# Kernel tuning notes

Hardware: AMD Instinct MI355X
Metric: run time of the kernel (lower is better)

Reference implementation:

```python
import jax, jax.numpy as jnp
import numpy as np

N = 50000      # nodes
E = 800000     # edges
C = 64         # in_channels
H = 192        # hidden_channels
ED = 16        # edge_dim
G = 2048       # num graphs (molecules)
L_EXTRA = 2    # num_layers - 1
T = 2          # num_timesteps
NEG0 = 0.2     # GATConv default negative_slope (first conv)
NEG = 0.01     # later convs / mol conv


def setup_inputs() -> dict:
    ks = iter(jax.random.split(jax.random.key(0), 48))
    def rn(shape, s=0.05):
        return jax.random.normal(next(ks), shape, dtype=jnp.float32) * s
    z = lambda *s: jnp.zeros(s, jnp.float32)
    return {
        "x": jax.random.normal(next(ks), (N, C), dtype=jnp.float32),
        "edge_index": jax.random.randint(next(ks), (2, E), 0, N),
        "edge_attr": jax.random.normal(next(ks), (E, ED), dtype=jnp.float32),
        "batch": jnp.sort(jax.random.randint(next(ks), (N,), 0, G)),
        "lin1_W": rn((H, C)), "lin1_b": z(H),
        "conv0_W": rn((H, H)), "conv0_att_s": rn((H,)), "conv0_att_d": rn((H,)),
        "conv0_We": rn((H, ED)), "conv0_att_e": rn((H,)), "conv0_b": z(H),
        "convs_W": rn((L_EXTRA, H, H)), "convs_att_s": rn((L_EXTRA, H)),
        "convs_att_d": rn((L_EXTRA, H)), "convs_b": z(L_EXTRA, H),
        "gru_Wih": rn((L_EXTRA + 1, 3 * H, H)), "gru_Whh": rn((L_EXTRA + 1, 3 * H, H)),
        "gru_bih": z(L_EXTRA + 1, 3 * H), "gru_bhh": z(L_EXTRA + 1, 3 * H),
        "mol_Wsrc": rn((H, H)), "mol_Wdst": rn((H, H)),
        "mol_att_s": rn((H,)), "mol_att_d": rn((H,)), "mol_b": z(H),
        "mgru_Wih": rn((3 * H, H)), "mgru_Whh": rn((3 * H, H)),
        "mgru_bih": z(3 * H), "mgru_bhh": z(3 * H),
        "lin2_W": rn((1, H)), "lin2_b": z(1),
    }


def _lrelu(v, slope):
    return jnp.where(v >= 0, v, slope * v)


def _seg_softmax(alpha, dst, n_seg):
    m = jax.ops.segment_max(alpha, dst, num_segments=n_seg)
    m = jnp.where(jnp.isfinite(m), m, 0.0)           # empty segments -> 0
    e = jnp.exp(alpha - m[dst])
    s = jax.ops.segment_sum(e, dst, num_segments=n_seg)
    return e / (s[dst] + 1e-16)


def _gat(h_src, h_dst, src, dst, att_s, att_d, b, slope, n_dst, alpha_extra=None):
    # h_src/h_dst are already linearly transformed node features
    alpha = (h_src * att_s).sum(-1)[src] + (h_dst * att_d).sum(-1)[dst]
    if alpha_extra is not None:
        alpha = alpha + alpha_extra
    w = _seg_softmax(_lrelu(alpha, slope), dst, n_dst)     # scatter-softmax over dst
    return jax.ops.segment_sum(h_src[src] * w[:, None], dst, num_segments=n_dst) + b


def _gru(h, hx, Wih, Whh, bih, bhh):
    gi = h @ Wih.T + bih
    gh = hx @ Whh.T + bhh
    ir, iz, inn = jnp.split(gi, 3, axis=-1)
    hr, hz, hn = jnp.split(gh, 3, axis=-1)
    r = jax.nn.sigmoid(ir + hr)
    zz = jax.nn.sigmoid(iz + hz)
    n = jnp.tanh(inn + r * hn)
    return (1.0 - zz) * n + zz * hx


def reference(x, edge_index, edge_attr, batch,
              lin1_W, lin1_b,
              conv0_W, conv0_att_s, conv0_att_d, conv0_We, conv0_att_e, conv0_b,
              convs_W, convs_att_s, convs_att_d, convs_b,
              gru_Wih, gru_Whh, gru_bih, gru_bhh,
              mol_Wsrc, mol_Wdst, mol_att_s, mol_att_d, mol_b,
              mgru_Wih, mgru_Whh, mgru_bih, mgru_bhh,
              lin2_W, lin2_b):
    src, dst = edge_index[0], edge_index[1]
    x = _lrelu(x @ lin1_W.T + lin1_b, 0.01)            # F.leaky_relu_ (slope 0.01)

    # ---- first GATConv: edge features + self loops (fill_value='mean') ----
    loop = jnp.arange(N)
    src0 = jnp.concatenate([src, loop])
    dst0 = jnp.concatenate([dst, loop])
    ea0 = jnp.concatenate([edge_attr, jnp.broadcast_to(edge_attr.mean(0), (N, ED))], 0)
    hW = x @ conv0_W.T                                  # shared lin_src/lin_dst
    alpha_e = (ea0 @ conv0_We.T * conv0_att_e).sum(-1)  # [E+N]
    h = jax.nn.elu(_gat(hW, hW, src0, dst0, conv0_att_s, conv0_att_d,
                        conv0_b, NEG0, N, alpha_e))
    x = jax.nn.relu(_gru(h, x, gru_Wih[0], gru_Whh[0], gru_bih[0], gru_bhh[0]))

    # ---- remaining atom GATConv + GRU layers ----
    for l in range(L_EXTRA):
        hW = x @ convs_W[l].T
        h = jax.nn.elu(_gat(hW, hW, src, dst, convs_att_s[l], convs_att_d[l],
                            convs_b[l], NEG, N))
        x = jax.nn.relu(_gru(h, x, gru_Wih[l + 1], gru_Whh[l + 1],
                             gru_bih[l + 1], gru_bhh[l + 1]))

    # ---- molecule readout: bipartite GAT (nodes -> molecules) + GRU ----
    out = jax.nn.relu(jax.ops.segment_sum(x, batch, num_segments=G))  # global_add_pool
    hs = x @ mol_Wsrc.T                                 # src transform (x fixed)
    node_ids = jnp.arange(N)
    for _ in range(T):
        hd = out @ mol_Wdst.T
        h = jax.nn.elu(_gat(hs, hd, node_ids, batch, mol_att_s, mol_att_d,
                            mol_b, NEG, G))
        out = jax.nn.relu(_gru(h, out, mgru_Wih, mgru_Whh, mgru_bih, mgru_bhh))

    return out @ lin2_W.T + lin2_b                      # [G, 1]
```

## Files before the change

kernel.cpp:

```cpp
#include <hip/hip_runtime.h>
#include <math.h>

#define NN    50000
#define EE    800000
#define CIN   64
#define HH    192
#define EDIM  16
#define GG    2048
#define H3    576
#define EA_BLOCKS 256
#define FRAG_ELEMS (36 * 6 * 64)
#define G4_WLAYER 221184

typedef _Float16 f16;
typedef _Float16 half8 __attribute__((ext_vector_type(8)));
typedef float f32x4 __attribute__((ext_vector_type(4)));

__device__ __forceinline__ unsigned fmap(float f) {
    unsigned u = __float_as_uint(f);
    return (u & 0x80000000u) ? ~u : (u | 0x80000000u);
}
__device__ __forceinline__ float funmap(unsigned u) {
    if (u == 0u) return 0.0f;
    return (u & 0x80000000u) ? __uint_as_float(u ^ 0x80000000u)
                             : __uint_as_float(~u);
}

__device__ __forceinline__ float fast_exp(float x) {
    return __builtin_amdgcn_exp2f(1.442695041f * x);
}
__device__ __forceinline__ float fast_sig(float x) {
    return __builtin_amdgcn_rcpf(1.f + __builtin_amdgcn_exp2f(-1.442695041f * x));
}
__device__ __forceinline__ float fast_tanh(float x) {
    return 1.f - 2.f * __builtin_amdgcn_rcpf(1.f + __builtin_amdgcn_exp2f(2.885390082f * x));
}
__device__ __forceinline__ float fast_expm1(float x) {
    return __builtin_amdgcn_exp2f(1.442695041f * x) - 1.f;
}

__device__ __forceinline__ void gload_lds16(const f16* g, f16* l) {
    __builtin_amdgcn_global_load_lds(
        (const __attribute__((address_space(1))) unsigned int*)g,
        (__attribute__((address_space(3))) unsigned int*)l,
        16, 0, 0);
}

__global__ void cvt_f2h(const float* __restrict__ s, f16* __restrict__ d, int n)
{
    int i = blockIdx.x * blockDim.x + threadIdx.x;
    if (i < n) d[i] = (f16)s[i];
}

struct Cvt8 { const float* s[8]; f16* d[8]; int n[8]; };
__global__ void cvt_multi(Cvt8 c)
{
    int slot = blockIdx.y;
    int i = blockIdx.x * blockDim.x + threadIdx.x;
    if (i < c.n[slot]) c.d[slot][i] = (f16)c.s[slot][i];
}

struct Pack8 { const f16* s[8]; f16* d[8]; };
__global__ __launch_bounds__(256) void pack_frag(Pack8 p)
{
    int slot = blockIdx.y;
    int idx = blockIdx.x * 256 + threadIdx.x;
    if (idx >= FRAG_ELEMS) return;
    int cb   = idx / 384;
    int rem  = idx % 384;
    int c    = rem / 64;
    int lane = rem % 64;
    int col = cb * 16 + (lane & 15);
    int k   = c * 32 + (lane >> 4) * 8;
    *(half8*)(p.d[slot] + (size_t)idx * 8) =
        *(const half8*)(p.s[slot] + (size_t)col * 192 + k);
}

__global__ __launch_bounds__(256) void pack4(const f16* __restrict__ Wih,
                                             const f16* __restrict__ Whh,
                                             f16* __restrict__ out)
{
    int layer = blockIdx.y;
    int idx = blockIdx.x * 256 + threadIdx.x;
    if (idx >= 27648) return;
    int frag = idx >> 6, lane = idx & 63;
    int pc6 = frag / 24, r24 = frag % 24;
    int p = pc6 / 6, c = pc6 % 6;
    int m = r24 / 12, g = (r24 % 12) >> 2, cb = r24 & 3;
    const f16* srcm = (m == 0 ? Wih : Whh) + (size_t)layer * (H3 * HH);
    int col = g * 192 + p * 64 + cb * 16 + (lane & 15);
    int k   = c * 32 + (lane >> 4) * 8;
    *(half8*)(out + (size_t)layer * G4_WLAYER + (size_t)idx * 8) =
        *(const half8*)(srcm + (size_t)col * 192 + k);
}

__global__ void hist_kernel(const int* __restrict__ idx, int* __restrict__ deg, int n, int nbins)
{
    int i = blockIdx.x * blockDim.x + threadIdx.x;
    if (i < n) {
        unsigned b = (unsigned)idx[i];
        if (b < (unsigned)nbins) atomicAdd(&deg[b], 1);
    }
}

__global__ void scan_wave(const int* __restrict__ deg, int* __restrict__ rowptr,
                          unsigned* __restrict__ cursor, int n)
{
    int lane = threadIdx.x & 63;
    int carry = 0;
    for (int base = 0; base < n; base += 64) {
        int i = base + lane;
        int v = (i < n) ? deg[i] : 0;
        int x = v;
        #pragma unroll
        for (int off = 1; off < 64; off <<= 1) {
            int t = __shfl_up(x, off);
            if (lane >= off) x += t;
        }
        int ex = carry + x - v;
        if (i < n) {
            rowptr[i] = ex;
            if (cursor) cursor[i] = (unsigned)ex;
        }
        carry += __shfl(x, 63);
    }
    if (lane == 0) rowptr[n] = carry;
}

__global__ __launch_bounds__(256) void chunk_sum(const int* __restrict__ deg,
                                                 int* __restrict__ csum, int n)
{
    int base = blockIdx.x * 1024;
    int tid = threadIdx.x;
    int i0 = base + tid * 4;
    int s = 0;
    #pragma unroll
    for (int k = 0; k < 4; k++) { int i = i0 + k; if (i < n) s += deg[i]; }
    #pragma unroll
    for (int off = 32; off > 0; off >>= 1) s += __shfl_down(s, off);
    __shared__ int ws[4];
    int lane = tid & 63, w = tid >> 6;
    if (lane == 0) ws[w] = s;
    __syncthreads();
    if (tid == 0) csum[blockIdx.x] = ws[0] + ws[1] + ws[2] + ws[3];
}

__global__ __launch_bounds__(256) void local_scan(const int* __restrict__ deg,
                                                  const int* __restrict__ choff,
                                                  int* __restrict__ rowptr,
                                                  unsigned* __restrict__ cursor,
                                                  int n, int nchunks)
{
    int base = blockIdx.x * 1024;
    int tid = threadIdx.x;
    int lane = tid & 63, w = tid >> 6;
    int i0 = base + tid * 4;
    int v[4];
    #pragma unroll
    for (int k = 0; k < 4; k++) { int i = i0 + k; v[k] = (i < n) ? deg[i] : 0; }
    int tsum = v[0] + v[1] + v[2] + v[3];
    int x = tsum;
    #pragma unroll
    for (int off = 1; off < 64; off <<= 1) {
        int t = __shfl_up(x, off);
        if (lane >= off) x += t;
    }
    __shared__ int wtot[4];
    if (lane == 63) wtot[w] = x;
    __syncthreads();
    int woff = 0;
    #pragma unroll
    for (int j = 0; j < 4; j++) if (j < w) woff += wtot[j];
    int ex = choff[blockIdx.x] + woff + x - tsum;
    #pragma unroll
    for (int k = 0; k < 4; k++) {
        int i = i0 + k;
        if (i < n) {
            rowptr[i] = ex;
            if (cursor) cursor[i] = (unsigned)ex;
        }
        ex += v[k];
    }
    if (blockIdx.x == 0 && tid == 0) rowptr[n] = choff[nchunks];
}

__global__ void scatter_kernel(const int* __restrict__ src, const int* __restrict__ dst,
                               unsigned* __restrict__ cursor,
                               int* __restrict__ csr_src, int* __restrict__ csr_eid, int E)
{
    int e = blockIdx.x * blockDim.x + threadIdx.x;
    if (e >= E) return;
    unsigned d = (unsigned)dst[e];
    if (d >= (unsigned)NN) return;
    unsigned p = atomicAdd(&cursor[d], 1u);
    if (p < (unsigned)E) {
        csr_src[p] = src[e];
        csr_eid[p] = e;
    }
}

__global__ __launch_bounds__(256) void gemm_mfma(const f16* __restrict__ A,
                                                 const f16* __restrict__ W,
                                                 const float* __restrict__ bias,
                                                 float* __restrict__ Cf,
                                                 f16* __restrict__ Ch,
                                                 int M, int N, int K, int act)
{
    __shared__ __align__(16) f16 sA[64 * 40];
    const int tid  = threadIdx.x;
    const int lane = tid & 63;
    const int wid  = tid >> 6;
    const int wy = wid >> 1, wx = wid & 1;
    const int m0 = blockIdx.x << 6, n0 = blockIdx.y << 6;
    const int n_ = lane & 15, quad = lane >> 4;

    f32x4 acc[2][2] = {};
    int boff0 = (n0 + wx * 32 + n_) * K + quad * 8;
    int boff1 = boff0 + 16 * K;

    const int srow = tid >> 2;
    const int skc  = (tid & 3) << 3;

    for (int k0 = 0; k0 < K; k0 += 32) {
        half8 av = {};
        int gm = m0 + srow;
        if (gm < M) av = *(const half8*)(A + (size_t)gm * K + k0 + skc);
        *(half8*)(sA + srow * 40 + skc) = av;
        __syncthreads();
        half8 a0 = *(const half8*)(sA + (wy * 32 + n_) * 40 + quad * 8);
        half8 a1 = *(const half8*)(sA + (wy * 32 + 16 + n_) * 40 + quad * 8);
        half8 b0 = *(const half8*)(W + boff0 + k0);
        half8 b1 = *(const half8*)(W + boff1 + k0);
        acc[0][0] = __builtin_amdgcn_mfma_f32_16x16x32_f16(a0, b0, acc[0][0], 0, 0, 0);
        acc[0][1] = __builtin_amdgcn_mfma_f32_16x16x32_f16(a0, b1, acc[0][1], 0, 0, 0);
        acc[1][0] = __builtin_amdgcn_mfma_f32_16x16x32_f16(a1, b0, acc[1][0], 0, 0, 0);
        acc[1][1] = __builtin_amdgcn_mfma_f32_16x16x32_f16(a1, b1, acc[1][1], 0, 0, 0);
        __syncthreads();
    }
    #pragma unroll
    for (int i = 0; i < 2; i++)
        #pragma unroll
        for (int j = 0; j < 2; j++) {
            int col = n0 + wx * 32 + j * 16 + n_;
            float bv = bias ? bias[col] : 0.f;
            #pragma unroll
            for (int reg = 0; reg < 4; reg++) {
                int row = m0 + wy * 32 + i * 16 + quad * 4 + reg;
                if (row >= M) continue;
                float v = acc[i][j][reg] + bv;
                if (act == 1) v = v >= 0.f ? v : 0.01f * v;
                if (Cf) Cf[(size_t)row * N + col] = v;
                if (Ch) Ch[(size_t)row * N + col] = (f16)v;
            }
        }
}

#define GRU_LDP 208
__global__ __launch_bounds__(256, 2) void gru_mfma(const f16* __restrict__ H16,
                                                   f16* __restrict__ X16,
                                                   const f16* __restrict__ Pih,
                                                   const f16* __restrict__ Phh,
                                                   const float* __restrict__ bih,
                                                   const float* __restrict__ bhh,
                                                   int M)
{
    __shared__ __align__(16) f16 sH[32 * GRU_LDP];
    __shared__ __align__(16) f16 sX[32 * GRU_LDP];
    const int tid  = threadIdx.x;
    const int lane = tid & 63;
    const int w    = tid >> 6;
    const int n_ = lane & 15, quad = lane >> 4;
    const int node0 = blockIdx.x << 5;

    {
        const int r  = tid >> 3;
        const int cb = (tid & 7) * 24;
        const int gm = node0 + r;
        if (gm < M) {
            const f16* hp = H16 + (size_t)gm * 192 + cb;
            const f16* xp = X16 + (size_t)gm * 192 + cb;
            #pragma unroll
            for (int q = 0; q < 3; q++) {
                *(half8*)(sH + r * GRU_LDP + cb + q * 8) = *(const half8*)(hp + q * 8);
                *(half8*)(sX + r * GRU_LDP + cb + q * 8) = *(const half8*)(xp + q * 8);
            }
        } else {
            half8 z = {};
            #pragma unroll
            for (int q = 0; q < 3; q++) {
                *(half8*)(sH + r * GRU_LDP + cb + q * 8) = z;
                *(half8*)(sX + r * GRU_LDP + cb + q * 8) = z;
            }
        }
    }
    __syncthreads();

    f32x4 aRZ[2][2][3] = {};
    f32x4 aIN[2][3] = {};
    f32x4 aHN[2][3] = {};
    int fb[3][3];
    #pragma unroll
    for (int g = 0; g < 3; g++)
        #pragma unroll
        for (int t = 0; t < 3; t++)
            fb[g][t] = (g * 12 + w * 3 + t) * 3072 + lane * 8;

    #pragma unroll 1
    for (int c = 0; c < 6; c++) {
        int k0 = c * 32;
        int po = c * 512;
        half8 ah0 = *(const half8*)(sH + n_ * GRU_LDP + k0 + quad * 8);
        half8 ah1 = *(const half8*)(sH + (16 + n_) * GRU_LDP + k0 + quad * 8);
        half8 ax0 = *(const half8*)(sX + n_ * GRU_LDP + k0 + quad * 8);
        half8 ax1 = *(const half8*)(sX + (16 + n_) * GRU_LDP + k0 + quad * 8);
        #pragma unroll
        for (int g = 0; g < 2; g++)
            #pragma unroll
            for (int t = 0; t < 3; t++) {
                half8 bI = *(const half8*)(Pih + fb[g][t] + po);
                half8 bH = *(const half8*)(Phh + fb[g][t] + po);
                aRZ[0][g][t] = __builtin_amdgcn_mfma_f32_16x16x32_f16(ah0, bI, aRZ[0][g][t], 0, 0, 0);
                aRZ[1][g][t] = __builtin_amdgcn_mfma_f32_16x16x32_f16(ah1, bI, aRZ[1][g][t], 0, 0, 0);
                aRZ[0][g][t] = __builtin_amdgcn_mfma_f32_16x16x32_f16(ax0, bH, aRZ[0][g][t], 0, 0, 0);
                aRZ[1][g][t] = __builtin_amdgcn_mfma_f32_16x16x32_f16(ax1, bH, aRZ[1][g][t], 0, 0, 0);
            }
        #pragma unroll
        for (int t = 0; t < 3; t++) {
            half8 bI = *(const half8*)(Pih + fb[2][t] + po);
            half8 bH = *(const half8*)(Phh + fb[2][t] + po);
            aIN[0][t] = __builtin_amdgcn_mfma_f32_16x16x32_f16(ah0, bI, aIN[0][t], 0, 0, 0);
            aIN[1][t] = __builtin_amdgcn_mfma_f32_16x16x32_f16(ah1, bI, aIN[1][t], 0, 0, 0);
            aHN[0][t] = __builtin_amdgcn_mfma_f32_16x16x32_f16(ax0, bH, aHN[0][t], 0, 0, 0);
            aHN[1][t] = __builtin_amdgcn_mfma_f32_16x16x32_f16(ax1, bH, aHN[1][t], 0, 0, 0);
        }
    }

    #pragma unroll
    for (int t = 0; t < 3; t++) {
        const int c0 = w * 48 + t * 16 + n_;
        float brz = bih[c0] + bhh[c0];
        float bzz = bih[c0 + 192] + bhh[c0 + 192];
        float bin = bih[c0 + 384], bhn = bhh[c0 + 384];
        #pragma unroll
        for (int half = 0; half < 2; half++) {
            #pragma unroll
            for (int reg = 0; reg < 4; reg++) {
                int rl = half * 16 + quad * 4 + reg;
                int node = node0 + rl;
                if (node >= M) continue;
                float hx = (float)sX[rl * GRU_LDP + c0];
                float r  = fast_sig(aRZ[half][0][t][reg] + brz);
                float z  = fast_sig(aRZ[half][1][t][reg] + bzz);
                float nn = fast_tanh(aIN[half][t][reg] + bin + r * (aHN[half][t][reg] + bhn));
                float o  = (1.f - z) * nn + z * hx;
                X16[(size_t)node * 192 + c0] = (f16)(o > 0.f ? o : 0.f);
            }
        }
    }
}

#define G4_ROWS 128
__global__ __launch_bounds__(256, 2) void gru4_mfma(const f16* __restrict__ H16,
                                                    const f16* __restrict__ Xold,
                                                    f16* __restrict__ Xnew,
                                                    const f16* __restrict__ W4,
                                                    const float* __restrict__ bih,
                                                    const float* __restrict__ bhh,
                                                    int M)
{
    __shared__ __align__(16) f16 sB[2][12288];
    const int tid  = threadIdx.x;
    const int lane = tid & 63;
    const int w    = tid >> 6;
    const int n_ = lane & 15, quad = lane >> 4;
    const int rb = blockIdx.x * G4_ROWS + w * 32;
    const int r0 = min(rb + n_,      M - 1);
    const int r1 = min(rb + 16 + n_, M - 1);

    half8 aA[4], aB[4];
    f32x4 acc[2][4][4] = {};

#define G4_STAGE(B, PC) do {                                                   \
        const f16* gs_ = W4 + (size_t)(PC) * 12288 + (w * 6) * 512 + lane * 8; \
        f16* ls_ = &sB[B][(w * 6) * 512];                                      \
        _Pragma("unroll")                                                      \
        for (int i_ = 0; i_ < 6; i_++)                                         \
            gload_lds16(gs_ + i_ * 512, ls_ + i_ * 512);                       \
    } while (0)

#define G4_ALOAD(AB, C) do {                                                   \
        const f16* h0_ = H16  + (size_t)r0 * 192 + (C) * 32 + quad * 8;        \
        const f16* h1_ = H16  + (size_t)r1 * 192 + (C) * 32 + quad * 8;        \
        const f16* x0_ = Xold + (size_t)r0 * 192 + (C) * 32 + quad * 8;        \
        const f16* x1_ = Xold + (size_t)r1 * 192 + (C) * 32 + quad * 8;        \
        AB[0] = *(const half8*)h0_;                                            \
        AB[1] = *(const half8*)h1_;                                            \
        AB[2] = *(const half8*)x0_;                                            \
        AB[3] = *(const half8*)x1_;                                            \
    } while (0)

#define G4_COMP(AB, CUR) do {                                                  \
        _Pragma("unroll")                                                      \
        for (int cb_ = 0; cb_ < 4; cb_++) {                                    \
            const f16* bp_ = &sB[CUR][cb_ * 512 + lane * 8];                   \
            half8 rI_ = *(const half8*)(bp_);                                  \
            half8 zI_ = *(const half8*)(bp_ + 2048);                           \
            half8 nI_ = *(const half8*)(bp_ + 4096);                           \
            half8 rH_ = *(const half8*)(bp_ + 6144);                           \
            half8 zH_ = *(const half8*)(bp_ + 8192);                           \
            half8 nH_ = *(const half8*)(bp_ + 10240);                          \
            acc[0][cb_][0] = __builtin_amdgcn_mfma_f32_16x16x32_f16(AB[0], rI_, acc[0][cb_][0], 0, 0, 0); \
            acc[0][cb_][0] = __builtin_amdgcn_mfma_f32_16x16x32_f16(AB[2], rH_, acc[0][cb_][0], 0, 0, 0); \
            acc[1][cb_][0] = __builtin_amdgcn_mfma_f32_16x16x32_f16(AB[1], rI_, acc[1][cb_][0], 0, 0, 0); \
            acc[1][cb_][0] = __builtin_amdgcn_mfma_f32_16x16x32_f16(AB[3], rH_, acc[1][cb_][0], 0, 0, 0); \
            acc[0][cb_][1] = __builtin_amdgcn_mfma_f32_16x16x32_f16(AB[0], zI_, acc[0][cb_][1], 0, 0, 0); \
            acc[0][cb_][1] = __builtin_amdgcn_mfma_f32_16x16x32_f16(AB[2], zH_, acc[0][cb_][1], 0, 0, 0); \
            acc[1][cb_][1] = __builtin_amdgcn_mfma_f32_16x16x32_f16(AB[1], zI_, acc[1][cb_][1], 0, 0, 0); \
            acc[1][cb_][1] = __builtin_amdgcn_mfma_f32_16x16x32_f16(AB[3], zH_, acc[1][cb_][1], 0, 0, 0); \
            acc[0][cb_][2] = __builtin_amdgcn_mfma_f32_16x16x32_f16(AB[0], nI_, acc[0][cb_][2], 0, 0, 0); \
            acc[1][cb_][2] = __builtin_amdgcn_mfma_f32_16x16x32_f16(AB[1], nI_, acc[1][cb_][2], 0, 0, 0); \
            acc[0][cb_][3] = __builtin_amdgcn_mfma_f32_16x16x32_f16(AB[2], nH_, acc[0][cb_][3], 0, 0, 0); \
            acc[1][cb_][3] = __builtin_amdgcn_mfma_f32_16x16x32_f16(AB[3], nH_, acc[1][cb_][3], 0, 0, 0); \
        }                                                                      \
    } while (0)

#define G4_EPI(P) do {                                                         \
        _Pragma("unroll")                                                      \
        for (int cb_ = 0; cb_ < 4; cb_++) {                                    \
            int c0_ = (P) * 64 + cb_ * 16 + n_;                                \
            float brz_ = bih[c0_] + bhh[c0_];                                  \
            float bzz_ = bih[c0_ + 192] + bhh[c0_ + 192];                      \
            float bin_ = bih[c0_ + 384], bhn_ = bhh[c0_ + 384];                \
            _Pragma("unroll")                                                  \
            for (int rh_ = 0; rh_ < 2; rh_++) {                                \
                _Pragma("unroll")                                              \
                for (int rg_ = 0; rg_ < 4; rg_++) {                            \
                    int node_ = rb + rh_ * 16 + quad * 4 + rg_;                \
                    if (node_ < M) {                                           \
                        float hx_ = (float)Xold[(size_t)node_ * 192 + c0_];    \
                        float r_  = fast_sig(acc[rh_][cb_][0][rg_] + brz_);    \
                        float z_  = fast_sig(acc[rh_][cb_][1][rg_] + bzz_);    \
                        float nn_ = fast_tanh(acc[rh_][cb_][2][rg_] + bin_ + r_ * (acc[rh_][cb_][3][rg_] + bhn_)); \
                        float o_  = (1.f - z_) * nn_ + z_ * hx_;               \
                        Xnew[(size_t)node_ * 192 + c0_] = (f16)(o_ > 0.f ? o_ : 0.f); \
                    }                                                          \
                    acc[rh_][cb_][0][rg_] = 0.f;                               \
                    acc[rh_][cb_][1][rg_] = 0.f;                               \
                    acc[rh_][cb_][2][rg_] = 0.f;                               \
                    acc[rh_][cb_][3][rg_] = 0.f;                               \
                }                                                              \
            }                                                                  \
        }                                                                      \
    } while (0)

#define G4_STEP(ACUR, ANXT, PC) do {                                           \
        if ((PC) < 17) {                                                       \
            G4_STAGE(((PC) + 1) & 1, (PC) + 1);                                \
            G4_ALOAD(ANXT, ((PC) + 1) % 6);                                    \
        }                                                                      \
        G4_COMP(ACUR, (PC) & 1);                                               \
        if (((PC) % 6) == 5) G4_EPI((PC) / 6);                                 \
        __syncthreads();                                                       \
    } while (0)

    G4_STAGE(0, 0);
    G4_ALOAD(aA, 0);
    __syncthreads();

    for (int pc = 0; pc < 18; pc += 2) {
        G4_STEP(aA, aB, pc);
        G4_STEP(aB, aA, pc + 1);
    }

#undef G4_STAGE
#undef G4_ALOAD
#undef G4_COMP
#undef G4_EPI
#undef G4_STEP
}

__global__ void compose_vec2(const float* __restrict__ W, const float* __restrict__ v,
                             float* __restrict__ out, int rows, int cols)
{
    int j = blockIdx.x * 4 + (threadIdx.x >> 6);
    if (j >= cols) return;
    int lane = threadIdx.x & 63;
    float acc = 0.f;
    for (int i = lane; i < rows; i += 64) acc += v[i] * W[(size_t)i * cols + j];
    #pragma unroll
    for (int off = 32; off > 0; off >>= 1) acc += __shfl_down(acc, off);
    if (lane == 0) out[j] = acc;
}

__global__ __launch_bounds__(256) void ea_sum_kernel(const float* __restrict__ ea,
                                                     float* __restrict__ partials, int E)
{
    __shared__ float ws[4][16];
    int tid = threadIdx.x;
    int lane = tid & 63, w = tid >> 6;
    float acc[16];
    #pragma unroll
    for (int f = 0; f < 16; f++) acc[f] = 0.f;
    for (int e = blockIdx.x * blockDim.x + tid; e < E; e += gridDim.x * blockDim.x) {
        const float4* p = (const float4*)(ea + (size_t)e * 16);
        float4 v0 = p[0], v1 = p[1], v2 = p[2], v3 = p[3];
        acc[0] += v0.x; acc[1] += v0.y; acc[2] += v0.z; acc[3] += v0.w;
        acc[4] += v1.x; acc[5] += v1.y; acc[6] += v1.z; acc[7] += v1.w;
        acc[8] += v2.x; acc[9] += v2.y; acc[10] += v2.z; acc[11] += v2.w;
        acc[12] += v3.x; acc[13] += v3.y; acc[14] += v3.z; acc[15] += v3.w;
    }
    #pragma unroll
    for (int off = 32; off > 0; off >>= 1)
        #pragma unroll
        for (int f = 0; f < 16; f++) acc[f] += __shfl_down(acc[f], off);
    if (lane == 0)
        #pragma unroll
        for (int f = 0; f < 16; f++) ws[w][f] = acc[f];
    __syncthreads();
    if (tid < 16)
        partials[blockIdx.x * 16 + tid] = ws[0][tid] + ws[1][tid] + ws[2][tid] + ws[3][tid];
}

__global__ void finalize_aloop(const float* __restrict__ partials, const float* __restrict__ ve,
                               float* __restrict__ aloop, float invE, int nblk)
{
    int tid = threadIdx.x;
    int total = nblk * 16;
    float vf = ve[tid & 15];
    float s = 0.f;
    for (int i = tid; i < total; i += 256) s += partials[i] * vf;
    #pragma unroll
    for (int off = 32; off > 0; off >>= 1) s += __shfl_down(s, off);
    __shared__ float ws[4];
    if ((tid & 63) == 0) ws[tid >> 6] = s;
    __syncthreads();
    if (tid == 0) *aloop = (ws[0] + ws[1] + ws[2] + ws[3]) * invE;
}

__global__ void row_dots_h(const f16* __restrict__ Mat, int M,
                           const float* __restrict__ v1, float* __restrict__ o1,
                           const float* __restrict__ v2, float* __restrict__ o2,
                           const float* __restrict__ bias)
{
    int row = blockIdx.x * 4 + (threadIdx.x >> 6);
    if (row >= M) return;
    int lane = threadIdx.x & 63;
    const f16* rp = Mat + (size_t)row * 192;
    float a1 = 0.f, a2 = 0.f;
    #pragma unroll
    for (int k = 0; k < 3; k++) {
        int f = lane + 64 * k;
        float x = (float)rp[f];
        a1 += x * v1[f];
        if (o2) a2 += x * v2[f];
    }
    #pragma unroll
    for (int off = 32; off > 0; off >>= 1) {
        a1 += __shfl_down(a1, off);
        a2 += __shfl_down(a2, off);
    }
    if (lane == 0) {
        o1[row] = a1 + (bias ? bias[0] : 0.f);
        if (o2) o2[row] = a2;
    }
}

__global__ void edge_alpha_max(const int* __restrict__ srcp, const int* __restrict__ dstp,
                               int E_real, int Etot,
                               const float* __restrict__ as_, const float* __restrict__ ad_,
                               const float* __restrict__ ea, const float* __restrict__ ve,
                               const float* __restrict__ aloop, float slope,
                               float* __restrict__ ab, unsigned* __restrict__ mb)
{
    int i = blockIdx.x * blockDim.x + threadIdx.x;
    if (i >= Etot) return;
    int s_, d_;
    float aext = 0.f;
    if (i < E_real) {
        s_ = srcp ? srcp[i] : i;
        d_ = dstp[i];
        if (ea) {
            const float4* p = (const float4*)(ea + (size_t)i * 16);
            const float4* q = (const float4*)ve;
            float4 e0 = p[0], e1 = p[1], e2 = p[2], e3 = p[3];
            float4 w0 = q[0], w1 = q[1], w2 = q[2], w3 = q[3];
            aext = e0.x * w0.x + e0.y * w0.y + e0.z * w0.z + e0.w * w0.w
                 + e1.x * w1.x + e1.y * w1.y + e1.z * w1.z + e1.w * w1.w
                 + e2.x * w2.x + e2.y * w2.y + e2.z * w2.z + e2.w * w2.w
                 + e3.x * w3.x + e3.y * w3.y + e3.z * w3.z + e3.w * w3.w;
        }
    } else {
        s_ = d_ = i - E_real;
        aext = *aloop;
    }
    float a = as_[s_] + ad_[d_] + aext;
    a = a >= 0.f ? a : slope * a;
    ab[i] = a;
    atomicMax(&mb[d_], fmap(a));
}

__global__ __launch_bounds__(256) void csr_aggregate(const int* __restrict__ rowptr,
                                                     const int* __restrict__ csr_src,
                                                     const int* __restrict__ csr_eid,
                                                     int Ndst, int nF, int nAb,
                                                     int selfloop, int selfAb,
                                                     const float* __restrict__ ab,
                                                     const unsigned* __restrict__ mb,
                                                     const f16* __restrict__ F,
                                                     const float* __restrict__ bias,
                                                     f16* __restrict__ Hout16)
{
    int node = blockIdx.x * 4 + (threadIdx.x >> 6);
    if (node >= Ndst) return;
    int lane = threadIdx.x & 63;
    int start = rowptr[node];
    int deg = rowptr[node + 1] - start;
    deg = min(max(deg, 0), 1 << 20);
    float m = funmap(mb[node]);

    float acc0 = 0.f, acc1 = 0.f, acc2 = 0.f, wsum = 0.f;
    for (int base = 0; base < deg; base += 64) {
        int i = base + lane;
        float wv = 0.f;
        int s = 0;
        if (i < deg) {
            int pos = start + i;
            s = csr_src ? csr_src[pos] : pos;
            if ((unsigned)s >= (unsigned)nF) s = 0;
            unsigned eid = csr_eid ? (unsigned)csr_eid[pos] : (unsigned)pos;
            if (eid >= (unsigned)nAb) eid = 0;
            wv = fast_exp(ab[eid] - m);
        }
        int cnt = min(64, deg - base);
        int j = 0;
        for (; j + 8 <= cnt; j += 8) {
            float wj[8];
            const f16* fp[8];
            #pragma unroll
            for (int q = 0; q < 8; q++) {
                wj[q] = __shfl(wv, j + q);
                fp[q] = F + (size_t)__shfl(s, j + q) * 192;
            }
            float a0[8], a1[8], a2[8];
            #pragma unroll
            for (int q = 0; q < 8; q++) {
                a0[q] = (float)fp[q][lane];
                a1[q] = (float)fp[q][lane + 64];
                a2[q] = (float)fp[q][lane + 128];
            }
            #pragma unroll
            for (int q = 0; q < 8; q++) {
                wsum += wj[q];
                acc0 += wj[q] * a0[q];
                acc1 += wj[q] * a1[q];
                acc2 += wj[q] * a2[q];
            }
        }
        for (; j < cnt; j++) {
            float wj = __shfl(wv, j);
            int   sj = __shfl(s, j);
            const f16* fr = F + (size_t)sj * 192;
            wsum += wj;
            acc0 += wj * (float)fr[lane];
            acc1 += wj * (float)fr[lane + 64];
            acc2 += wj * (float)fr[lane + 128];
        }
    }
    if (selfloop) {
        unsigned eid = (unsigned)(selfAb + node);
        float wv = (eid < (unsigned)nAb) ? fast_exp(ab[eid] - m) : 0.f;
        int s = min(node, nF - 1);
        const f16* fr = F + (size_t)s * 192;
        wsum += wv;
        acc0 += wv * (float)fr[lane];
        acc1 += wv * (float)fr[lane + 64];
        acc2 += wv * (float)fr[lane + 128];
    }
    float inv = 1.f / (wsum + 1e-16f);
    float h0 = acc0 * inv + bias[lane];
    float h1 = acc1 * inv + bias[lane + 64];
    float h2 = acc2 * inv + bias[lane + 128];
    f16* orow = Hout16 + (size_t)node * 192;
    orow[lane]       = (f16)(h0 > 0.f ? h0 : fast_expm1(h0));
    orow[lane + 64]  = (f16)(h1 > 0.f ? h1 : fast_expm1(h1));
    orow[lane + 128] = (f16)(h2 > 0.f ? h2 : fast_expm1(h2));
}

__global__ void pool_csr(const int* __restrict__ brow, const f16* __restrict__ X,
                         f16* __restrict__ outg16, int G)
{
    int g = blockIdx.x * 4 + (threadIdx.x >> 6);
    if (g >= G) return;
    int lane = threadIdx.x & 63;
    float a0 = 0.f, a1 = 0.f, a2 = 0.f;
    int s = max(brow[g], 0);
    int e = min(brow[g + 1], NN);
    for (int n = s; n < e; n++) {
        const f16* xr = X + (size_t)n * 192;
        a0 += (float)xr[lane];
        a1 += (float)xr[lane + 64];
        a2 += (float)xr[lane + 128];
    }
    f16* o = outg16 + (size_t)g * 192;
    o[lane]       = (f16)(a0 > 0.f ? a0 : 0.f);
    o[lane + 64]  = (f16)(a1 > 0.f ? a1 : 0.f);
    o[lane + 128] = (f16)(a2 > 0.f ? a2 : 0.f);
}

extern "C" void kernel_launch(void* const* d_in, const int* in_sizes, int n_in,
                              void* d_out, int out_size, void* d_ws, size_t ws_size,
                              hipStream_t stream)
{
    const float* x_in        = (const float*)d_in[0];
    const int*   ei          = (const int*)  d_in[1];
    const float* eattr       = (const float*)d_in[2];
    const int*   batch       = (const int*)  d_in[3];
    const float* lin1_W      = (const float*)d_in[4];
    const float* lin1_b      = (const float*)d_in[5];
    const float* conv0_W     = (const float*)d_in[6];
    const float* conv0_att_s = (const float*)d_in[7];
    const float* conv0_att_d = (const float*)d_in[8];
    const float* conv0_We    = (const float*)d_in[9];
    const float* conv0_att_e = (const float*)d_in[10];
    const float* conv0_b     = (const float*)d_in[11];
    const float* convs_W     = (const float*)d_in[12];
    const float* convs_att_s = (const float*)d_in[13];
    const float* convs_att_d = (const float*)d_in[14];
    const float* convs_b     = (const float*)d_in[15];
    const float* gru_Wih     = (const float*)d_in[16];
    const float* gru_Whh     = (const float*)d_in[17];
    const float* gru_bih     = (const float*)d_in[18];
    const float* gru_bhh     = (const float*)d_in[19];
    const float* mol_Wsrc    = (const float*)d_in[20];
    const float* mol_Wdst    = (const float*)d_in[21];
    const float* mol_att_s   = (const float*)d_in[22];
    const float* mol_att_d   = (const float*)d_in[23];
    const float* mol_b       = (const float*)d_in[24];
    const float* mgru_Wih    = (const float*)d_in[25];
    const float* mgru_Whh    = (const float*)d_in[26];
    const float* mgru_bih    = (const float*)d_in[27];
    const float* mgru_bhh    = (const float*)d_in[28];
    const float* lin2_W      = (const float*)d_in[29];
    const float* lin2_b      = (const float*)d_in[30];

    const int* src = ei;
    const int* dst = ei + EE;

    char* base = (char*)d_ws;
    size_t off = 0;
    auto alloc = [&](size_t bytes) -> void* {
        void* p = base + off;
        off = (off + bytes + 63) & ~(size_t)63;
        return p;
    };
    f16*      w16    = (f16*)alloc((size_t)NN * HH * 2);
    f16*      h16    = (f16*)alloc((size_t)NN * HH * 2);
    f16*      x16    = (f16*)alloc((size_t)NN * HH * 2);
    f16*      x16b   = (f16*)alloc((size_t)NN * HH * 2);
    f16*      xin16  = (f16*)alloc((size_t)NN * CIN * 2);
    float*    abuf   = (float*)alloc((size_t)(EE + NN) * 4);
    float*    asb    = (float*)alloc((size_t)NN * 4);
    float*    adb    = (float*)alloc((size_t)NN * 4);
    unsigned* mb     = (unsigned*)alloc((size_t)NN * 4);
    f16*      hg16   = (f16*)alloc((size_t)GG * HH * 2);
    f16*      outg16 = (f16*)alloc((size_t)GG * HH * 2);
    float*    adg    = (float*)alloc((size_t)GG * 4);
    unsigned* mg     = (unsigned*)alloc((size_t)GG * 4);
    int*      degb   = (int*)alloc((size_t)NN * 4);
    int*      rowptr = (int*)alloc((size_t)(NN + 1) * 4);
    unsigned* cursor = (unsigned*)alloc((size_t)NN * 4);
    int*      csr_src = (int*)alloc((size_t)EE * 4);
    int*      csr_eid = (int*)alloc((size_t)EE * 4);
    int*      bdeg   = (int*)alloc((size_t)GG * 4);
    int*      brow   = (int*)alloc((size_t)(GG + 1) * 4);
    int*      csum   = (int*)alloc(64 * 4);
    int*      choff  = (int*)alloc(65 * 4);
    float*    ve     = (float*)alloc(64);
    float*    eapart = (float*)alloc((size_t)EA_BLOCKS * 16 * 4);
    float*    vd     = (float*)alloc(HH * 4);
    float*    aloop  = (float*)alloc(64);
    f16*      lin1W16   = (f16*)alloc((size_t)HH * CIN * 2);
    f16*      conv0W16  = (f16*)alloc((size_t)HH * HH * 2);
    f16*      convsW16  = (f16*)alloc((size_t)2 * HH * HH * 2);
    f16*      gruWih16  = (f16*)alloc((size_t)3 * H3 * HH * 2);
    f16*      gruWhh16  = (f16*)alloc((size_t)3 * H3 * HH * 2);
    f16*      molWs16   = (f16*)alloc((size_t)HH * HH * 2);
    f16*      mgruWih16 = (f16*)alloc((size_t)H3 * HH * 2);
    f16*      mgruWhh16 = (f16*)alloc((size_t)H3 * HH * 2);
    f16*      gruWihP   = (f16*)alloc((size_t)3 * FRAG_ELEMS * 8 * 2);
    f16*      gruWhhP   = (f16*)alloc((size_t)3 * FRAG_ELEMS * 8 * 2);
    f16*      mgruWihP  = (f16*)alloc((size_t)FRAG_ELEMS * 8 * 2);
    f16*      mgruWhhP  = (f16*)alloc((size_t)FRAG_ELEMS * 8 * 2);
    f16*      gru4W     = (f16*)alloc((size_t)3 * G4_WLAYER * 2);
    if (off > ws_size) return;

    cvt_f2h<<<(NN * CIN + 255) / 256, 256, 0, stream>>>(x_in, xin16, NN * CIN);
    Cvt8 cv;
    cv.s[0] = lin1_W;   cv.d[0] = lin1W16;   cv.n[0] = HH * CIN;
    cv.s[1] = conv0_W;  cv.d[1] = conv0W16;  cv.n[1] = HH * HH;
    cv.s[2] = convs_W;  cv.d[2] = convsW16;  cv.n[2] = 2 * HH * HH;
    cv.s[3] = gru_Wih;  cv.d[3] = gruWih16;  cv.n[3] = 3 * H3 * HH;
    cv.s[4] = gru_Whh;  cv.d[4] = gruWhh16;  cv.n[4] = 3 * H3 * HH;
    cv.s[5] = mol_Wsrc; cv.d[5] = molWs16;   cv.n[5] = HH * HH;
    cv.s[6] = mgru_Wih; cv.d[6] = mgruWih16; cv.n[6] = H3 * HH;
    cv.s[7] = mgru_Whh; cv.d[7] = mgruWhh16; cv.n[7] = H3 * HH;
    cvt_multi<<<dim3((3 * H3 * HH + 255) / 256, 8), 256, 0, stream>>>(cv);

    Pack8 pk;
    const size_t WM = (size_t)H3 * HH;
    pk.s[0] = gruWih16;            pk.d[0] = gruWihP;
    pk.s[1] = gruWih16 + WM;       pk.d[1] = gruWihP + WM;
    pk.s[2] = gruWih16 + 2 * WM;   pk.d[2] = gruWihP + 2 * WM;
    pk.s[3] = gruWhh16;            pk.d[3] = gruWhhP;
    pk.s[4] = gruWhh16 + WM;       pk.d[4] = gruWhhP + WM;
    pk.s[5] = gruWhh16 + 2 * WM;   pk.d[5] = gruWhhP + 2 * WM;
    pk.s[6] = mgruWih16;           pk.d[6] = mgruWihP;
    pk.s[7] = mgruWhh16;           pk.d[7] = mgruWhhP;
    pack_frag<<<dim3((FRAG_ELEMS + 255) / 256, 8), 256, 0, stream>>>(pk);

    pack4<<<dim3(108, 3), 256, 0, stream>>>(gruWih16, gruWhh16, gru4W);

    const int nchunks = (NN + 1023) / 1024;
    hipMemsetAsync(degb, 0, NN * sizeof(int), stream);
    hist_kernel<<<(EE + 255) / 256, 256, 0, stream>>>(dst, degb, EE, NN);
    chunk_sum<<<nchunks, 256, 0, stream>>>(degb, csum, NN);
    scan_wave<<<1, 64, 0, stream>>>(csum, choff, nullptr, nchunks);
    local_scan<<<nchunks, 256, 0, stream>>>(degb, choff, rowptr, cursor, NN, nchunks);
    scatter_kernel<<<(EE + 255) / 256, 256, 0, stream>>>(src, dst, cursor, csr_src, csr_eid, EE);
    hipMemsetAsync(bdeg, 0, GG * sizeof(int), stream);
    hist_kernel<<<(NN + 255) / 256, 256, 0, stream>>>(batch, bdeg, NN, GG);
    chunk_sum<<<2, 256, 0, stream>>>(bdeg, csum, GG);
    scan_wave<<<1, 64, 0, stream>>>(csum, choff, nullptr, 2);
    local_scan<<<2, 256, 0, stream>>>(bdeg, choff, brow, nullptr, GG, 2);

    compose_vec2<<<(EDIM + 3) / 4, 256, 0, stream>>>(conv0_We, conv0_att_e, ve, HH, EDIM);
    ea_sum_kernel<<<EA_BLOCKS, 256, 0, stream>>>(eattr, eapart, EE);
    finalize_aloop<<<1, 256, 0, stream>>>(eapart, ve, aloop, 1.0f / EE, EA_BLOCKS);

    const dim3 gemmGrid((NN + 63) / 64, HH / 64);
    const int g4grid = (NN + G4_ROWS - 1) / G4_ROWS;

    f16* xcur = x16;
    f16* xnxt = x16b;

    gemm_mfma<<<gemmGrid, 256, 0, stream>>>(xin16, lin1W16, lin1_b, nullptr, xcur, NN, HH, CIN, 1);

    gemm_mfma<<<gemmGrid, 256, 0, stream>>>(xcur, conv0W16, nullptr, nullptr, w16, NN, HH, HH, 0);
    row_dots_h<<<(NN + 3) / 4, 256, 0, stream>>>(w16, NN, conv0_att_s, asb, conv0_att_d, adb, nullptr);
    hipMemsetAsync(mb, 0, NN * 4, stream);
    edge_alpha_max<<<(EE + NN + 255) / 256, 256, 0, stream>>>(src, dst, EE, EE + NN, asb, adb,
                                                              eattr, ve, aloop, 0.2f, abuf, mb);
    csr_aggregate<<<(NN + 3) / 4, 256, 0, stream>>>(rowptr, csr_src, csr_eid, NN, NN, EE + NN,
                                                    1, EE, abuf, mb, w16, conv0_b, h16);
    gru4_mfma<<<g4grid, 256, 0, stream>>>(h16, xcur, xnxt, gru4W, gru_bih, gru_bhh, NN);
    { f16* tmp = xcur; xcur = xnxt; xnxt = tmp; }

    for (int l = 0; l < 2; l++) {
        gemm_mfma<<<gemmGrid, 256, 0, stream>>>(xcur, convsW16 + (size_t)l * HH * HH,
                                                nullptr, nullptr, w16, NN, HH, HH, 0);
        row_dots_h<<<(NN + 3) / 4, 256, 0, stream>>>(w16, NN, convs_att_s + l * HH, asb,
                                                     convs_att_d + l * HH, adb, nullptr);
        hipMemsetAsync(mb, 0, NN * 4, stream);
        edge_alpha_max<<<(EE + 255) / 256, 256, 0, stream>>>(src, dst, EE, EE, asb, adb,
                                                             nullptr, nullptr, nullptr, 0.01f, abuf, mb);
        csr_aggregate<<<(NN + 3) / 4, 256, 0, stream>>>(rowptr, csr_src, csr_eid, NN, NN, EE,
                                                        0, 0, abuf, mb, w16, convs_b + l * HH, h16);
        gru4_mfma<<<g4grid, 256, 0, stream>>>(h16, xcur, xnxt,
                                              gru4W + (size_t)(l + 1) * G4_WLAYER,
                                              gru_bih + (size_t)(l + 1) * H3,
                                              gru_bhh + (size_t)(l + 1) * H3, NN);
        { f16* tmp = xcur; xcur = xnxt; xnxt = tmp; }
    }

    pool_csr<<<(GG + 3) / 4, 256, 0, stream>>>(brow, xcur, outg16, GG);
    gemm_mfma<<<gemmGrid, 256, 0, stream>>>(xcur, molWs16, nullptr, nullptr, w16, NN, HH, HH, 0);
    row_dots_h<<<(NN + 3) / 4, 256, 0, stream>>>(w16, NN, mol_att_s, asb, nullptr, nullptr, nullptr);
    compose_vec2<<<(HH + 3) / 4, 256, 0, stream>>>(mol_Wdst, mol_att_d, vd, HH, HH);

    for (int t = 0; t < 2; t++) {
        row_dots_h<<<(GG + 3) / 4, 256, 0, stream>>>(outg16, GG, vd, adg, nullptr, nullptr, nullptr);
        hipMemsetAsync(mg, 0, GG * 4, stream);
        edge_alpha_max<<<(NN + 255) / 256, 256, 0, stream>>>(nullptr, batch, NN, NN, asb, adg,
                                                             nullptr, nullptr, nullptr, 0.01f, abuf, mg);
        csr_aggregate<<<(GG + 3) / 4, 256, 0, stream>>>(brow, nullptr, nullptr, GG, NN, NN,
                                                        0, 0, abuf, mg, w16, mol_b, hg16);
        gru_mfma<<<(GG + 31) / 32, 256, 0, stream>>>(hg16, outg16, mgruWihP, mgruWhhP,
                                                     mgru_bih, mgru_bhh, GG);
    }

    row_dots_h<<<(GG + 3) / 4, 256, 0, stream>>>(outg16, GG, lin2_W, (float*)d_out,
                                                 nullptr, nullptr, lin2_b);
}
```

Measured before the change: 1.054 ms.

## Fuse edge attention scores into CSR aggregation with online softmax

Removes the separate edge_alpha_max kernel, its atomicMax segment-max buffer and the memsets. Each wavefront now computes the attention logits for its destination node's CSR edges on the fly and uses a running max with rescaling, as in online softmax. This avoids writing and rereading the per-edge alpha buffer and the scattered atomics. In exchange, the first layer gathers edge attributes by edge id inside the aggregation, and each 64-edge chunk adds a wave-wide max reduction.

Measured after the change: 905.9 us. 14.1% less time.

```diff
diff --git a/kernel.cpp b/kernel.cpp
--- a/kernel.cpp
+++ b/kernel.cpp
@@ -15,16 +15,6 @@
 typedef _Float16 f16;
 typedef _Float16 half8 __attribute__((ext_vector_type(8)));
 typedef float f32x4 __attribute__((ext_vector_type(4)));
-
-__device__ __forceinline__ unsigned fmap(float f) {
-    unsigned u = __float_as_uint(f);
-    return (u & 0x80000000u) ? ~u : (u | 0x80000000u);
-}
-__device__ __forceinline__ float funmap(unsigned u) {
-    if (u == 0u) return 0.0f;
-    return (u & 0x80000000u) ? __uint_as_float(u ^ 0x80000000u)
-                             : __uint_as_float(~u);
-}
 
 __device__ __forceinline__ float fast_exp(float x) {
     return __builtin_amdgcn_exp2f(1.442695041f * x);
@@ -565,47 +555,16 @@
     }
 }
 
-__global__ void edge_alpha_max(const int* __restrict__ srcp, const int* __restrict__ dstp,
-                               int E_real, int Etot,
-                               const float* __restrict__ as_, const float* __restrict__ ad_,
-                               const float* __restrict__ ea, const float* __restrict__ ve,
-                               const float* __restrict__ aloop, float slope,
-                               float* __restrict__ ab, unsigned* __restrict__ mb)
-{
-    int i = blockIdx.x * blockDim.x + threadIdx.x;
-    if (i >= Etot) return;
-    int s_, d_;
-    float aext = 0.f;
-    if (i < E_real) {
-        s_ = srcp ? srcp[i] : i;
-        d_ = dstp[i];
-        if (ea) {
-            const float4* p = (const float4*)(ea + (size_t)i * 16);
-            const float4* q = (const float4*)ve;
-            float4 e0 = p[0], e1 = p[1], e2 = p[2], e3 = p[3];
-            float4 w0 = q[0], w1 = q[1], w2 = q[2], w3 = q[3];
-            aext = e0.x * w0.x + e0.y * w0.y + e0.z * w0.z + e0.w * w0.w
-                 + e1.x * w1.x + e1.y * w1.y + e1.z * w1.z + e1.w * w1.w
-                 + e2.x * w2.x + e2.y * w2.y + e2.z * w2.z + e2.w * w2.w
-                 + e3.x * w3.x + e3.y * w3.y + e3.z * w3.z + e3.w * w3.w;
-        }
-    } else {
-        s_ = d_ = i - E_real;
-        aext = *aloop;
-    }
-    float a = as_[s_] + ad_[d_] + aext;
-    a = a >= 0.f ? a : slope * a;
-    ab[i] = a;
-    atomicMax(&mb[d_], fmap(a));
-}
-
 __global__ __launch_bounds__(256) void csr_aggregate(const int* __restrict__ rowptr,
                                                      const int* __restrict__ csr_src,
                                                      const int* __restrict__ csr_eid,
-                                                     int Ndst, int nF, int nAb,
-                                                     int selfloop, int selfAb,
-                                                     const float* __restrict__ ab,
-                                                     const unsigned* __restrict__ mb,
+                                                     int Ndst, int nF,
+                                                     int selfloop, float slope,
+                                                     const float* __restrict__ as_,
+                                                     const float* __restrict__ ad_,
+                                                     const float* __restrict__ ea,
+                                                     const float* __restrict__ ve,
+                                                     const float* __restrict__ aloop,
                                                      const f16* __restrict__ F,
                                                      const float* __restrict__ bias,
                                                      f16* __restrict__ Hout16)
@@ -616,21 +575,43 @@
     int start = rowptr[node];
     int deg = rowptr[node + 1] - start;
     deg = min(max(deg, 0), 1 << 20);
-    float m = funmap(mb[node]);
-
+    float adn = ad_[node];
+
+    float m = -INFINITY;
     float acc0 = 0.f, acc1 = 0.f, acc2 = 0.f, wsum = 0.f;
     for (int base = 0; base < deg; base += 64) {
         int i = base + lane;
-        float wv = 0.f;
+        float a = -INFINITY;
         int s = 0;
         if (i < deg) {
             int pos = start + i;
             s = csr_src ? csr_src[pos] : pos;
             if ((unsigned)s >= (unsigned)nF) s = 0;
-            unsigned eid = csr_eid ? (unsigned)csr_eid[pos] : (unsigned)pos;
-            if (eid >= (unsigned)nAb) eid = 0;
-            wv = fast_exp(ab[eid] - m);
-        }
+            float aext = 0.f;
+            if (ea) {
+                unsigned eid = (unsigned)csr_eid[pos];
+                if (eid >= (unsigned)EE) eid = 0;
+                const float4* p = (const float4*)(ea + (size_t)eid * 16);
+                const float4* q = (const float4*)ve;
+                float4 e0 = p[0], e1 = p[1], e2 = p[2], e3 = p[3];
+                float4 w0 = q[0], w1 = q[1], w2 = q[2], w3 = q[3];
+                aext = e0.x * w0.x + e0.y * w0.y + e0.z * w0.z + e0.w * w0.w
+                     + e1.x * w1.x + e1.y * w1.y + e1.z * w1.z + e1.w * w1.w
+                     + e2.x * w2.x + e2.y * w2.y + e2.z * w2.z + e2.w * w2.w
+                     + e3.x * w3.x + e3.y * w3.y + e3.z * w3.z + e3.w * w3.w;
+            }
+            a = as_[s] + adn + aext;
+            a = a >= 0.f ? a : slope * a;
+        }
+        float cm = a;
+        #pragma unroll
+        for (int off = 32; off > 0; off >>= 1) cm = fmaxf(cm, __shfl_xor(cm, off));
+        float mn = fmaxf(m, cm);
+        float sc = fast_exp(m - mn);
+        acc0 *= sc; acc1 *= sc; acc2 *= sc; wsum *= sc;
+        m = mn;
+        float wv = fast_exp(a - m);
+
         int cnt = min(64, deg - base);
         int j = 0;
         for (; j + 8 <= cnt; j += 8) {
@@ -667,8 +648,12 @@
         }
     }
     if (selfloop) {
-        unsigned eid = (unsigned)(selfAb + node);
-        float wv = (eid < (unsigned)nAb) ? fast_exp(ab[eid] - m) : 0.f;
+        float a = as_[node] + adn + *aloop;
+        a = a >= 0.f ? a : slope * a;
+        float mn = fmaxf(m, a);
+        float sc = fast_exp(m - mn);
+        acc0 *= sc; acc1 *= sc; acc2 *= sc; wsum *= sc;
+        float wv = fast_exp(a - mn);
         int s = min(node, nF - 1);
         const f16* fr = F + (size_t)s * 192;
         wsum += wv;
@@ -758,14 +743,11 @@
     f16*      x16    = (f16*)alloc((size_t)NN * HH * 2);
     f16*      x16b   = (f16*)alloc((size_t)NN * HH * 2);
     f16*      xin16  = (f16*)alloc((size_t)NN * CIN * 2);
-    float*    abuf   = (float*)alloc((size_t)(EE + NN) * 4);
     float*    asb    = (float*)alloc((size_t)NN * 4);
     float*    adb    = (float*)alloc((size_t)NN * 4);
-    unsigned* mb     = (unsigned*)alloc((size_t)NN * 4);
     f16*      hg16   = (f16*)alloc((size_t)GG * HH * 2);
     f16*      outg16 = (f16*)alloc((size_t)GG * HH * 2);
     float*    adg    = (float*)alloc((size_t)GG * 4);
-    unsigned* mg     = (unsigned*)alloc((size_t)GG * 4);
     int*      degb   = (int*)alloc((size_t)NN * 4);
     int*      rowptr = (int*)alloc((size_t)(NN + 1) * 4);
     unsigned* cursor = (unsigned*)alloc((size_t)NN * 4);
@@ -847,11 +829,9 @@
 
     gemm_mfma<<<gemmGrid, 256, 0, stream>>>(xcur, conv0W16, nullptr, nullptr, w16, NN, HH, HH, 0);
     row_dots_h<<<(NN + 3) / 4, 256, 0, stream>>>(w16, NN, conv0_att_s, asb, conv0_att_d, adb, nullptr);
-    hipMemsetAsync(mb, 0, NN * 4, stream);
-    edge_alpha_max<<<(EE + NN + 255) / 256, 256, 0, stream>>>(src, dst, EE, EE + NN, asb, adb,
-                                                              eattr, ve, aloop, 0.2f, abuf, mb);
-    csr_aggregate<<<(NN + 3) / 4, 256, 0, stream>>>(rowptr, csr_src, csr_eid, NN, NN, EE + NN,
-                                                    1, EE, abuf, mb, w16, conv0_b, h16);
+    csr_aggregate<<<(NN + 3) / 4, 256, 0, stream>>>(rowptr, csr_src, csr_eid, NN, NN,
+                                                    1, 0.2f, asb, adb, eattr, ve, aloop,
+                                                    w16, conv0_b, h16);
     gru4_mfma<<<g4grid, 256, 0, stream>>>(h16, xcur, xnxt, gru4W, gru_bih, gru_bhh, NN);
     { f16* tmp = xcur; xcur = xnxt; xnxt = tmp; }
 
@@ -860,11 +840,9 @@
                                                 nullptr, nullptr, w16, NN, HH, HH, 0);
         row_dots_h<<<(NN + 3) / 4, 256, 0, stream>>>(w16, NN, convs_att_s + l * HH, asb,
                                                      convs_att_d + l * HH, adb, nullptr);
-        hipMemsetAsync(mb, 0, NN * 4, stream);
-        edge_alpha_max<<<(EE + 255) / 256, 256, 0, stream>>>(src, dst, EE, EE, asb, adb,
-                                                             nullptr, nullptr, nullptr, 0.01f, abuf, mb);
-        csr_aggregate<<<(NN + 3) / 4, 256, 0, stream>>>(rowptr, csr_src, csr_eid, NN, NN, EE,
-                                                        0, 0, abuf, mb, w16, convs_b + l * HH, h16);
+        csr_aggregate<<<(NN + 3) / 4, 256, 0, stream>>>(rowptr, csr_src, csr_eid, NN, NN,
+                                                        0, 0.01f, asb, adb, nullptr, nullptr, nullptr,
+                                                        w16, convs_b + l * HH, h16);
         gru4_mfma<<<g4grid, 256, 0, stream>>>(h16, xcur, xnxt,
                                               gru4W + (size_t)(l + 1) * G4_WLAYER,
                                               gru_bih + (size_t)(l + 1) * H3,
@@ -879,11 +857,9 @@
 
     for (int t = 0; t < 2; t++) {
         row_dots_h<<<(GG + 3) / 4, 256, 0, stream>>>(outg16, GG, vd, adg, nullptr, nullptr, nullptr);
-        hipMemsetAsync(mg, 0, GG * 4, stream);
-        edge_alpha_max<<<(NN + 255) / 256, 256, 0, stream>>>(nullptr, batch, NN, NN, asb, adg,
-                                                             nullptr, nullptr, nullptr, 0.01f, abuf, mg);
-        csr_aggregate<<<(GG + 3) / 4, 256, 0, stream>>>(brow, nullptr, nullptr, GG, NN, NN,
-                                                        0, 0, abuf, mg, w16, mol_b, hg16);
+        csr_aggregate<<<(GG + 3) / 4, 256, 0, stream>>>(brow, nullptr, nullptr, GG, NN,
+                                                        0, 0.01f, asb, adg, nullptr, nullptr, nullptr,
+                                                        w16, mol_b, hg16);
         gru_mfma<<<(GG + 31) / 32, 256, 0, stream>>>(hg16, outg16, mgruWihP, mgruWhhP,
                                                      mgru_bih, mgru_bhh, GG);
     }
```
